# Optimization experiments

Measured on AMD Instinct MI355X. Metric: run time of the kernel, lower is better.

The kernel has to match this reference:

```python
import jax, jax.numpy as jnp
import numpy as np

N, E, B, IN = 20000, 320000, 64, 192


def setup_inputs() -> dict:
    key = jax.random.key(0)
    ks = iter(jax.random.split(key, 80))
    d = {}
    d["x"] = jax.random.normal(next(ks), (N, IN), jnp.float32)
    d["edge_index"] = jax.random.randint(next(ks), (2, E), 0, N - 1)  # +1 shift stays < N
    d["edge_attr"] = jax.random.normal(next(ks), (E,), jnp.float32)
    d["batch"] = jnp.sort(jax.random.randint(next(ks), (N,), 0, B))

    def lin(i, o):
        w = jax.random.normal(next(ks), (i, o), jnp.float32) * (1.0 / i ** 0.5)
        return w, jnp.zeros((o,), jnp.float32)

    dims = [(IN, 4, 64), (256, 4, 64), (256, 6, 32)]  # (in_ch, heads, out_ch) per conv
    for l, (ic, h, c) in enumerate(dims, 1):
        hc = h * c
        d[f"Wq{l}"], d[f"bq{l}"] = lin(ic, hc)
        d[f"Wk{l}"], d[f"bk{l}"] = lin(ic, hc)
        d[f"Wv{l}"], d[f"bv{l}"] = lin(ic, hc)
        d[f"We{l}"] = jax.random.normal(next(ks), (1, hc), jnp.float32)  # lin_edge, no bias
        d[f"Ws{l}"], d[f"bs{l}"] = lin(ic, hc)  # root/skip weight
    d["g1"] = jnp.ones((256,), jnp.float32); d["be1"] = jnp.zeros((256,), jnp.float32)
    d["g2"] = jnp.ones((256,), jnp.float32); d["be2"] = jnp.zeros((256,), jnp.float32)
    d["fc1_w"], d["fc1_b"] = lin(192, 32)
    d["fc2_w"], d["fc2_b"] = lin(32, 2)
    return d


def seg_softmax(s, seg, n):
    # per-destination-node softmax over edges, [E, H]
    m = jax.ops.segment_max(s, seg, num_segments=n)
    m = jnp.where(jnp.isfinite(m), m, 0.0)
    ex = jnp.exp(s - m[seg])
    den = jax.ops.segment_sum(ex, seg, num_segments=n)
    return ex / (den[seg] + 1e-16)


def tconv(x, src, dst, e, Wq, bq, Wk, bk, Wv, bv, We, Ws, bs, h, c):
    # PyG TransformerConv (concat=True, root_weight=True, beta=False, eval -> no dropout)
    n = x.shape[0]
    q = (x @ Wq + bq).reshape(n, h, c)
    k = (x @ Wk + bk).reshape(n, h, c)
    v = (x @ Wv + bv).reshape(n, h, c)
    ee = (e @ We).reshape(-1, h, c)           # [E, h, c] edge embedding
    kj = k[src] + ee                           # gather keys along edges
    scores = jnp.einsum('ehc,ehc->eh', q[dst], kj) * (1.0 / c ** 0.5)
    alpha = seg_softmax(scores, dst, n)        # [E, h]
    msg = (v[src] + ee) * alpha[..., None]
    out = jax.ops.segment_sum(msg, dst, num_segments=n).reshape(n, h * c)
    return out + x @ Ws + bs, alpha


def ln(x, g, b):
    mu = x.mean(-1, keepdims=True)
    var = x.var(-1, keepdims=True)
    return g * (x - mu) / jnp.sqrt(var + 1e-5) + b


def _forward(x, edge_index, edge_attr, batch, Wq1, bq1, Wk1, bk1, Wv1, bv1, We1, Ws1, bs1, Wq2, bq2, Wk2, bk2, Wv2, bv2, We2, Ws2, bs2, Wq3, bq3, Wk3, bk3, Wv3, bv3, We3, Ws3, bs3, g1, be1, g2, be2, fc1_w, fc1_b, fc2_w, fc2_b):
    ei = edge_index + 1                       # replicates `edge_index += 1` in source
    src, dst = ei[0], ei[1]
    e = edge_attr[:, None]                    # edge_dim = 1
    x1, a1 = tconv(x, src, dst, e, Wq1, bq1, Wk1, bk1, Wv1, bv1, We1, Ws1, bs1, 4, 64)
    x1 = jax.nn.relu(ln(x1, g1, be1))
    x2, a2 = tconv(x1, src, dst, e, Wq2, bq2, Wk2, bk2, Wv2, bv2, We2, Ws2, bs2, 4, 64)
    x2 = jax.nn.relu(ln(x2, g2, be2))
    x3, a3 = tconv(x2, src, dst, e, Wq3, bq3, Wk3, bk3, Wv3, bv3, We3, Ws3, bs3, 6, 32)
    x3 = jax.nn.relu(x3)                      # note: norm3 exists in __init__ but is never applied
    xr = x + x3
    cnt = jax.ops.segment_sum(jnp.ones((xr.shape[0],), xr.dtype), batch, num_segments=B)
    pooled = jax.ops.segment_sum(xr, batch, num_segments=B) / jnp.maximum(cnt, 1.0)[:, None]
    h = jax.nn.relu(pooled @ fc1_w + fc1_b)
    logits = h @ fc2_w + fc2_b
    return logits, a1, a2, a3


def reference(x, edge_index, edge_attr, batch, Wq1, bq1, Wk1, bk1, Wv1, bv1, We1, Ws1, bs1, Wq2, bq2, Wk2, bk2, Wv2, bv2, We2, Ws2, bs2, Wq3, bq3, Wk3, bk3, Wv3, bv3, We3, Ws3, bs3, g1, be1, g2, be2, fc1_w, fc1_b, fc2_w, fc2_b):
    return _forward(x, edge_index, edge_attr, batch, Wq1, bq1, Wk1, bk1, Wv1, bv1, We1, Ws1, bs1, Wq2, bq2, Wk2, bk2, Wv2, bv2, We2, Ws2, bs2, Wq3, bq3, Wk3, bk3, Wv3, bv3, We3, Ws3, bs3, g1, be1, g2, be2, fc1_w, fc1_b, fc2_w, fc2_b)
```

## Files before the change

kernel.cpp:

```cpp
#include <hip/hip_runtime.h>
#include <cstdint>
#include <cstddef>

#define DEVINL __device__ __forceinline__

typedef short s16x8 __attribute__((ext_vector_type(8)));
typedef float f32x4 __attribute__((ext_vector_type(4)));
typedef unsigned short u16x4 __attribute__((ext_vector_type(4)));
typedef unsigned short u16x8 __attribute__((ext_vector_type(8)));

DEVINL unsigned short f2bf(float f) {
  unsigned u = __float_as_uint(f);
  unsigned r = (u + 0x7FFFu + ((u >> 16) & 1u)) >> 16;
  return (unsigned short)r;
}
DEVINL float bf2f(unsigned short b) { return __uint_as_float(((unsigned)b) << 16); }

__global__ __launch_bounds__(256) void fill_i32(int* __restrict__ p, int val, int n) {
  int i = blockIdx.x * 256 + threadIdx.x;
  if (i < n) p[i] = val;
}


__global__ __launch_bounds__(256) void cvt_split(const float* __restrict__ in,
                                                 unsigned short* __restrict__ hi,
                                                 unsigned short* __restrict__ lo, int n) {
  int i = blockIdx.x * 256 + threadIdx.x;
  if (i >= n) return;
  float f = in[i];
  unsigned short h = f2bf(f);
  float r = f - bf2f(h);
  hi[i] = h;
  lo[i] = f2bf(r);
}

struct CvtWArgs {
  const float* W[12];
  int K[12];
  int M[12];
};
__global__ __launch_bounds__(256) void cvt_w_all(CvtWArgs a,
                                                 unsigned short* __restrict__ Wh,
                                                 unsigned short* __restrict__ Wl) {
  int tid = blockIdx.x * 256 + threadIdx.x;
  int mat = tid >> 16;
  int off = tid & 65535;
  if (mat >= 12) return;
  int K = a.K[mat], M = a.M[mat];
  if (off >= K * M) return;
  int k = off / M, m = off - k * M;
  float f = a.W[mat][off];
  unsigned short h = f2bf(f);
  float r = f - bf2f(h);
  size_t dst = (size_t)mat * 65536 + (size_t)m * K + k;
  Wh[dst] = h;
  Wl[dst] = f2bf(r);
}

struct GemmArgs {
  const unsigned short* Wh[4];
  const unsigned short* Wl[4];
  const float* bias[4];
  float* out[4];
  int obf[4];
};

template <int KTOT>
__global__ __launch_bounds__(256, 3) void gemm4_lds(
    const unsigned short* __restrict__ Ah, const unsigned short* __restrict__ Al,
    GemmArgs args, int N, int M) {
  const int BK = 64;
  __shared__ unsigned short ash[128 * 64];
  __shared__ unsigned short asl[128 * 64];
  __shared__ unsigned short wsh[64 * 64];
  __shared__ unsigned short wsl[64 * 64];
  int tid = threadIdx.x;
  int wave = tid >> 6, lane = tid & 63;
  int lrow = lane & 15, quad = lane >> 4;
  int mt = M >> 6;
  int z = blockIdx.x / mt;
  int colTile = blockIdx.x - z * mt;
  int row0 = blockIdx.y * 128;
  int col0 = colTile * 64;
  const unsigned short* __restrict__ Wh = args.Wh[z];
  const unsigned short* __restrict__ Wl = args.Wl[z];
  const bool full = (args.obf[z] == 0);

  int ar[4], asq[4];
  size_t agoff[4];
#pragma unroll
  for (int i = 0; i < 4; i++) {
    int c = tid + i * 256;
    ar[i] = c >> 3;
    int kq = c & 7;
    asq[i] = kq ^ (ar[i] & 7);
    int gr = row0 + ar[i]; if (gr >= N) gr = N - 1;
    agoff[i] = (size_t)gr * KTOT + kq * 8;
  }
  int wr[2], wsq[2];
  size_t wgoff[2];
#pragma unroll
  for (int i = 0; i < 2; i++) {
    int c = tid + i * 256;
    wr[i] = c >> 3;
    int kq = c & 7;
    wsq[i] = kq ^ (wr[i] & 7);
    wgoff[i] = (size_t)(col0 + wr[i]) * KTOT + kq * 8;
  }

  s16x8 pa_h[4], pa_l[4], pw_h[2], pw_l[2];
#pragma unroll
  for (int i = 0; i < 4; i++) {
    pa_h[i] = *(const s16x8*)(Ah + agoff[i]);
    pa_l[i] = *(const s16x8*)(Al + agoff[i]);
  }
#pragma unroll
  for (int i = 0; i < 2; i++) {
    pw_h[i] = *(const s16x8*)(Wh + wgoff[i]);
    if (full) pw_l[i] = *(const s16x8*)(Wl + wgoff[i]);
  }

  f32x4 acc[2][4] = {};

  for (int k0 = 0; k0 < KTOT; k0 += BK) {
    __syncthreads();
#pragma unroll
    for (int i = 0; i < 4; i++) {
      *(s16x8*)(ash + ar[i] * 64 + asq[i] * 8) = pa_h[i];
      *(s16x8*)(asl + ar[i] * 64 + asq[i] * 8) = pa_l[i];
    }
#pragma unroll
    for (int i = 0; i < 2; i++) {
      *(s16x8*)(wsh + wr[i] * 64 + wsq[i] * 8) = pw_h[i];
      if (full) *(s16x8*)(wsl + wr[i] * 64 + wsq[i] * 8) = pw_l[i];
    }
    if (k0 + BK < KTOT) {
      int kn = k0 + BK;
#pragma unroll
      for (int i = 0; i < 4; i++) {
        pa_h[i] = *(const s16x8*)(Ah + agoff[i] + kn);
        pa_l[i] = *(const s16x8*)(Al + agoff[i] + kn);
      }
#pragma unroll
      for (int i = 0; i < 2; i++) {
        pw_h[i] = *(const s16x8*)(Wh + wgoff[i] + kn);
        if (full) pw_l[i] = *(const s16x8*)(Wl + wgoff[i] + kn);
      }
    }
    __syncthreads();
#pragma unroll
    for (int kk = 0; kk < 2; kk++) {
      s16x8 fah[2], fal[2], fbh[4], fbl[4];
#pragma unroll
      for (int rf = 0; rf < 2; rf++) {
        int r = wave * 32 + rf * 16 + lrow;
        int sq = (kk * 4 + quad) ^ (lrow & 7);
        fah[rf] = *(const s16x8*)(ash + r * 64 + sq * 8);
        fal[rf] = *(const s16x8*)(asl + r * 64 + sq * 8);
      }
#pragma unroll
      for (int cf = 0; cf < 4; cf++) {
        int cc = cf * 16 + lrow;
        int sq = (kk * 4 + quad) ^ (lrow & 7);
        fbh[cf] = *(const s16x8*)(wsh + cc * 64 + sq * 8);
        if (full) fbl[cf] = *(const s16x8*)(wsl + cc * 64 + sq * 8);
      }
#pragma unroll
      for (int rf = 0; rf < 2; rf++)
#pragma unroll
        for (int cf = 0; cf < 4; cf++) {
          acc[rf][cf] = __builtin_amdgcn_mfma_f32_16x16x32_bf16(fah[rf], fbh[cf], acc[rf][cf], 0, 0, 0);
          acc[rf][cf] = __builtin_amdgcn_mfma_f32_16x16x32_bf16(fal[rf], fbh[cf], acc[rf][cf], 0, 0, 0);
          if (full)
            acc[rf][cf] = __builtin_amdgcn_mfma_f32_16x16x32_bf16(fah[rf], fbl[cf], acc[rf][cf], 0, 0, 0);
        }
    }
  }
  const float* __restrict__ bias = args.bias[z];
  int obf = args.obf[z];
  if (obf == 0) {
    float* __restrict__ C = args.out[z];
#pragma unroll
    for (int cf = 0; cf < 4; cf++) {
      int col = col0 + cf * 16 + lrow;
      float bv = bias[col];
#pragma unroll
      for (int rf = 0; rf < 2; rf++) {
        int rb = row0 + wave * 32 + rf * 16 + quad * 4;
#pragma unroll
        for (int r = 0; r < 4; r++) {
          int rr = rb + r;
          if (rr < N) C[(size_t)rr * M + col] = acc[rf][cf][r] + bv;
        }
      }
    }
  } else {
    __syncthreads();
#pragma unroll
    for (int cf = 0; cf < 4; cf++) {
      int col = cf * 16 + lrow;
      float bv = bias[col0 + col];
#pragma unroll
      for (int rf = 0; rf < 2; rf++) {
        int rl = wave * 32 + rf * 16 + quad * 4;
#pragma unroll
        for (int r = 0; r < 4; r++)
          ash[(rl + r) * 64 + col] = f2bf(acc[rf][cf][r] + bv);
      }
    }
    __syncthreads();
    unsigned short* __restrict__ C = (unsigned short*)args.out[z];
    if (obf == 1) {
#pragma unroll
      for (int i = 0; i < 4; i++) {
        int c = tid + i * 256;
        int row = c >> 3, g8 = c & 7;
        int rr = row0 + row;
        if (rr < N)
          *(u16x8*)(C + (size_t)rr * M + col0 + g8 * 8) =
              *(const u16x8*)(ash + row * 64 + g8 * 8);
      }
    } else {
      int voff = (obf == 3) ? 4 : 0;
      int gbase = col0 >> 2;
#pragma unroll
      for (int i = 0; i < 8; i++) {
        int c = tid + i * 256;
        int row = c >> 4, g4 = c & 15;
        int rr = row0 + row;
        if (rr < N)
          *(u16x4*)(C + (size_t)rr * 2 * M + (size_t)(gbase + g4) * 8 + voff) =
              *(const u16x4*)(ash + row * 64 + g4 * 4);
      }
    }
  }
}


__global__ __launch_bounds__(256) void hist_dst(const int* __restrict__ dst,
                                                int* __restrict__ cnt, int E) {
  int e = blockIdx.x * 256 + threadIdx.x;
  if (e < E) atomicAdd(&cnt[dst[e] + 1], 1);
}

__global__ __launch_bounds__(1024) void scan_hist(const int* __restrict__ cnt,
                                                  int* __restrict__ start,
                                                  int* __restrict__ off, int N) {
  __shared__ int sums[1024];
  const int CH = 20;
  int t = threadIdx.x;
  int base = t * CH;
  int local[CH];
  int tot = 0;
  if (base < N) {
#pragma unroll
    for (int i = 0; i < CH; i++) { local[i] = cnt[base + i]; tot += local[i]; }
  }
  sums[t] = tot;
  __syncthreads();
  for (int d = 1; d < 1024; d <<= 1) {
    int v = (t >= d) ? sums[t - d] : 0;
    __syncthreads();
    sums[t] += v;
    __syncthreads();
  }
  if (base < N) {
    int run = (t == 0) ? 0 : sums[t - 1];
#pragma unroll
    for (int i = 0; i < CH; i++) { start[base + i] = run; off[base + i] = run; run += local[i]; }
    if (base + CH == N) start[N] = run;
  }
}

__global__ __launch_bounds__(256) void scatter_edges(
    const int* __restrict__ src, const int* __restrict__ dst,
    const float* __restrict__ ea, int* __restrict__ off,
    int* __restrict__ src_s, float* __restrict__ ea_s, int* __restrict__ eid_s, int E) {
  int e = blockIdx.x * 256 + threadIdx.x;
  if (e >= E) return;
  int d = dst[e] + 1;
  int pos = atomicAdd(&off[d], 1);
  src_s[pos] = src[e] + 1;
  ea_s[pos] = ea[e];
  eid_s[pos] = e;
}

template <int H, int LPH>
__global__ __launch_bounds__(256) void attn_fused(
    const unsigned short* __restrict__ q, const unsigned short* __restrict__ kv,
    const float* __restrict__ We,
    const int* __restrict__ start, const int* __restrict__ src_s,
    const float* __restrict__ ea_s, const int* __restrict__ eid_s,
    float* __restrict__ sc, float* __restrict__ outp,
    float* __restrict__ alpha, int Nn, float scale) {
  const int HC = H * LPH * 4;
  int w = (blockIdx.x * 256 + threadIdx.x) >> 6;
  int lane = threadIdx.x & 63;
  if (w >= Nn) return;
  int b = start[w], e = start[w + 1];
  if (b == e) return;
  bool act = lane < H * LPH;
  int idx = lane * 4;
  int head = lane / LPH;
  float4 q4 = make_float4(0.f, 0.f, 0.f, 0.f), We4 = q4;
  if (act) {
    u16x4 qv = *(const u16x4*)(q + (size_t)w * HC + idx);
    q4.x = bf2f(qv.x); q4.y = bf2f(qv.y); q4.z = bf2f(qv.z); q4.w = bf2f(qv.w);
    We4 = *(const float4*)(We + idx);
  }
  float qwe = q4.x * We4.x + q4.y * We4.y + q4.z * We4.z + q4.w * We4.w;
#pragma unroll
  for (int mm = 1; mm < LPH; mm <<= 1) qwe += __shfl_xor(qwe, mm, 64);

  float l = 0.f, tv = 0.f;
  float4 accv = make_float4(0.f, 0.f, 0.f, 0.f);

  auto step = [&](u16x8 kvv, float eav, int pos) {
    float p = q4.x * bf2f(kvv[0]) + q4.y * bf2f(kvv[1]) +
              q4.z * bf2f(kvv[2]) + q4.w * bf2f(kvv[3]);
#pragma unroll
    for (int mm = 1; mm < LPH; mm <<= 1) p += __shfl_xor(p, mm, 64);
    float es = __expf((p + eav * qwe) * scale);
    if (act && (lane % LPH) == 0) sc[(size_t)pos * H + head] = es;
    l += es;
    tv = fmaf(es, eav, tv);
    accv.x = fmaf(es, bf2f(kvv[4]), accv.x);
    accv.y = fmaf(es, bf2f(kvv[5]), accv.y);
    accv.z = fmaf(es, bf2f(kvv[6]), accv.z);
    accv.w = fmaf(es, bf2f(kvv[7]), accv.w);
  };

  u16x8 z8 = {0, 0, 0, 0, 0, 0, 0, 0};
  u16x8 kvS[4] = {z8, z8, z8, z8};
  float eaS[4] = {0.f, 0.f, 0.f, 0.f};

  auto preload = [&](int pos, int st) {
    int s = src_s[pos]; eaS[st] = ea_s[pos];
    if (act) kvS[st] = *(const u16x8*)(kv + (size_t)s * 2 * HC + lane * 8);
  };

#pragma unroll
  for (int j = 0; j < 4; j++) if (b + j < e) preload(b + j, j);

  for (int pos = b; pos < e; pos += 4) {
#pragma unroll
    for (int j = 0; j < 4; j++) {
      if (pos + j < e) {
        u16x8 kvc = kvS[j];
        float ec = eaS[j];
        if (pos + j + 4 < e) preload(pos + j + 4, j);
        step(kvc, ec, pos + j);
      }
    }
  }

  float invl = 1.0f / (l + 1e-16f);
  if (act) {
    float* orow = outp + (size_t)w * HC + idx;
    float4 o = *(float4*)orow;
    o.x += (accv.x + tv * We4.x) * invl;
    o.y += (accv.y + tv * We4.y) * invl;
    o.z += (accv.z + tv * We4.z) * invl;
    o.w += (accv.w + tv * We4.w) * invl;
    *(float4*)orow = o;
  }
  {
    int len = e - b;
    const int PCH = 64 / H;
    int p_of = lane / H;
    int h_of = lane - p_of * H;
    float myinv = __shfl(invl, h_of * LPH, 64);
    __threadfence_block();
    for (int base = 0; base < len; base += PCH) {
      int po = base + p_of;
      if (p_of < PCH && po < len) {
        int pos = b + po;
        float es = sc[(size_t)pos * H + h_of];
        alpha[(size_t)eid_s[pos] * H + h_of] = es * myinv;
      }
    }
  }
}


__global__ __launch_bounds__(256) void ln_relu_split(
    const float* __restrict__ in, const float* __restrict__ g,
    const float* __restrict__ b, unsigned short* __restrict__ hi,
    unsigned short* __restrict__ lo, int N) {
  int w = (blockIdx.x * 256 + threadIdx.x) >> 6;
  int lane = threadIdx.x & 63;
  if (w >= N) return;
  float4 x = *(const float4*)(in + (size_t)w * 256 + lane * 4);
  float s = x.x + x.y + x.z + x.w;
  float s2 = x.x * x.x + x.y * x.y + x.z * x.z + x.w * x.w;
  for (int m = 1; m < 64; m <<= 1) { s += __shfl_xor(s, m, 64); s2 += __shfl_xor(s2, m, 64); }
  float mu = s * (1.0f / 256.0f);
  float var = s2 * (1.0f / 256.0f) - mu * mu;
  float inv = rsqrtf(var + 1e-5f);
  float4 gv = *(const float4*)(g + lane * 4);
  float4 bv = *(const float4*)(b + lane * 4);
  float4 y;
  y.x = fmaxf(fmaf((x.x - mu) * inv, gv.x, bv.x), 0.f);
  y.y = fmaxf(fmaf((x.y - mu) * inv, gv.y, bv.y), 0.f);
  y.z = fmaxf(fmaf((x.z - mu) * inv, gv.z, bv.z), 0.f);
  y.w = fmaxf(fmaf((x.w - mu) * inv, gv.w, bv.w), 0.f);
  u16x4 yh, yl;
  yh.x = f2bf(y.x); yl.x = f2bf(y.x - bf2f(yh.x));
  yh.y = f2bf(y.y); yl.y = f2bf(y.y - bf2f(yh.y));
  yh.z = f2bf(y.z); yl.z = f2bf(y.z - bf2f(yh.z));
  yh.w = f2bf(y.w); yl.w = f2bf(y.w - bf2f(yh.w));
  *(u16x4*)(hi + (size_t)w * 256 + lane * 4) = yh;
  *(u16x4*)(lo + (size_t)w * 256 + lane * 4) = yl;
}

__global__ __launch_bounds__(192) void resid_pool2(
    const float* __restrict__ x, const float* __restrict__ x3,
    const int* __restrict__ batch, float* __restrict__ pooled,
    float* __restrict__ cnt, int N, int R) {
  int col = threadIdx.x;
  int r0 = blockIdx.x * R;
  int r1 = min(r0 + R, N);
  if (r0 >= N) return;
  float acc = 0.f;
  int cur = batch[r0];
  int run = 0;
  for (int r = r0; r < r1; r++) {
    int b = batch[r];
    if (b != cur) {
      atomicAdd(&pooled[cur * 192 + col], acc);
      if (col == 0) atomicAdd(&cnt[cur], (float)run);
      acc = 0.f; run = 0; cur = b;
    }
    size_t i = (size_t)r * 192 + col;
    acc += x[i] + fmaxf(x3[i], 0.f);
    run++;
  }
  atomicAdd(&pooled[cur * 192 + col], acc);
  if (col == 0) atomicAdd(&cnt[cur], (float)run);
}

__global__ __launch_bounds__(64) void head_mlp(
    const float* __restrict__ pooled, const float* __restrict__ cnt,
    const float* __restrict__ fc1w, const float* __restrict__ fc1b,
    const float* __restrict__ fc2w, const float* __restrict__ fc2b,
    float* __restrict__ logits) {
  int b = blockIdx.x;
  int t = threadIdx.x;
  __shared__ float p[192];
  __shared__ float hbuf[32];
  float inv = 1.0f / fmaxf(cnt[b], 1.0f);
  for (int i = t; i < 192; i += 64) p[i] = pooled[b * 192 + i] * inv;
  __syncthreads();
  if (t < 32) {
    float acc = fc1b[t];
    for (int i = 0; i < 192; i++) acc = fmaf(p[i], fc1w[i * 32 + t], acc);
    hbuf[t] = fmaxf(acc, 0.f);
  }
  __syncthreads();
  if (t < 2) {
    float acc = fc2b[t];
    for (int j = 0; j < 32; j++) acc = fmaf(hbuf[j], fc2w[j * 2 + t], acc);
    logits[b * 2 + t] = acc;
  }
}

static inline int divup(int a, int b) { return (a + b - 1) / b; }

extern "C" void kernel_launch(void* const* d_in, const int* in_sizes, int n_in,
                              void* d_out, int out_size, void* d_ws, size_t ws_size,
                              hipStream_t stream) {
  const int N = 20000, E = 320000, B = 64;
  const float* x     = (const float*)d_in[0];
  const int*   ei    = (const int*)d_in[1];
  const float* eattr = (const float*)d_in[2];
  const int*   batch = (const int*)d_in[3];
  const int* srcp = ei;
  const int* dstp = ei + E;

  const float* Wq[3]; const float* bq[3]; const float* Wk[3]; const float* bk[3];
  const float* Wv[3]; const float* bv[3]; const float* We[3]; const float* Ws[3];
  const float* bs[3];
  for (int l = 0; l < 3; l++) {
    int base = 4 + l * 9;
    Wq[l] = (const float*)d_in[base + 0]; bq[l] = (const float*)d_in[base + 1];
    Wk[l] = (const float*)d_in[base + 2]; bk[l] = (const float*)d_in[base + 3];
    Wv[l] = (const float*)d_in[base + 4]; bv[l] = (const float*)d_in[base + 5];
    We[l] = (const float*)d_in[base + 6];
    Ws[l] = (const float*)d_in[base + 7]; bs[l] = (const float*)d_in[base + 8];
  }
  const float* g1  = (const float*)d_in[31]; const float* be1 = (const float*)d_in[32];
  const float* g2  = (const float*)d_in[33]; const float* be2 = (const float*)d_in[34];
  const float* fc1w = (const float*)d_in[35]; const float* fc1b = (const float*)d_in[36];
  const float* fc2w = (const float*)d_in[37]; const float* fc2b = (const float*)d_in[38];

  float* out = (float*)d_out;
  float* logits = out;
  float* a1 = out + 128;
  float* a2 = a1 + (size_t)E * 4;
  float* a3 = a2 + (size_t)E * 4;

  float* ws = (float*)d_ws;
  size_t o = 0;
  float* qb = ws + o; o += (size_t)N * 256;
  float* kvb = ws + o; o += (size_t)N * 256;
  float* xa = ws + o; o += (size_t)N * 256;
  float* xb = ws + o; o += (size_t)N * 256;
  float* sc = ws + o; o += (size_t)E * 6;
  int*   cntb  = (int*)(ws + o); o += N;
  int*   startb= (int*)(ws + o); o += N + 1;
  int*   offb  = (int*)(ws + o); o += N + 1;
  int*   src_s = (int*)(ws + o); o += E;
  float* ea_s  = ws + o; o += E;
  int*   eid_s = (int*)(ws + o); o += E;
  float* pooled = ws + o; o += (size_t)B * 192;
  float* cnt    = ws + o; o += B;
  unsigned short* Ah = (unsigned short*)(ws + o); o += (size_t)N * 128;
  unsigned short* Al = (unsigned short*)(ws + o); o += (size_t)N * 128;
  unsigned short* Wh12 = (unsigned short*)(ws + o); o += (size_t)12 * 32768;
  unsigned short* Wl12 = (unsigned short*)(ws + o); o += (size_t)12 * 32768;

  unsigned short* qh  = (unsigned short*)qb;
  unsigned short* kvh = (unsigned short*)kvb;

  dim3 blk(256);

  struct LayerCfg { int K, M; float scale; };
  LayerCfg cfg[3] = {
    {192, 256, 0.125f},
    {256, 256, 0.125f},
    {256, 192, 0.1767766952966369f},
  };
  CvtWArgs cwa;
  for (int l = 0; l < 3; l++) {
    cwa.W[l * 4 + 0] = Wq[l]; cwa.W[l * 4 + 1] = Wk[l];
    cwa.W[l * 4 + 2] = Wv[l]; cwa.W[l * 4 + 3] = Ws[l];
    for (int zz = 0; zz < 4; zz++) {
      cwa.K[l * 4 + zz] = cfg[l].K; cwa.M[l * 4 + zz] = cfg[l].M;
    }
  }
  cvt_w_all<<<12 * 65536 / 256, blk, 0, stream>>>(cwa, Wh12, Wl12);

  fill_i32<<<divup(N, 256), blk, 0, stream>>>(cntb, 0, N);
  hist_dst<<<divup(E, 256), blk, 0, stream>>>(dstp, cntb, E);
  scan_hist<<<1, dim3(1024), 0, stream>>>(cntb, startb, offb, N);
  scatter_edges<<<divup(E, 256), blk, 0, stream>>>(srcp, dstp, eattr, offb,
                                                  src_s, ea_s, eid_s, E);

  float*       lay_out[3] = {xa, xb, xa};
  float*       alpha_out[3] = {a1, a2, a3};

  cvt_split<<<divup(N * 192, 256), blk, 0, stream>>>(x, Ah, Al, N * 192);

  for (int l = 0; l < 3; l++) {
    int M = cfg[l].M;
    GemmArgs ga;
    float* outs[4] = {(float*)qh, (float*)kvh, (float*)kvh, lay_out[l]};
    const float* biases[4] = {bq[l], bk[l], bv[l], bs[l]};
    int obfs[4] = {1, 2, 3, 0};
    for (int z = 0; z < 4; z++) {
      ga.Wh[z] = Wh12 + (size_t)(l * 4 + z) * 65536;
      ga.Wl[z] = Wl12 + (size_t)(l * 4 + z) * 65536;
      ga.bias[z] = biases[z];
      ga.out[z] = outs[z];
      ga.obf[z] = obfs[z];
    }
    dim3 gg((M >> 6) * 4, divup(N, 128));
    if (l == 0)      gemm4_lds<192><<<gg, blk, 0, stream>>>(Ah, Al, ga, N, M);
    else             gemm4_lds<256><<<gg, blk, 0, stream>>>(Ah, Al, ga, N, M);

    dim3 gat(divup(N * 64, 256));
    if (l < 2) {
      attn_fused<4, 16><<<gat, blk, 0, stream>>>(qh, kvh, We[l], startb, src_s,
                                                 ea_s, eid_s, sc, lay_out[l],
                                                 alpha_out[l], N, cfg[l].scale);
    } else {
      attn_fused<6, 8><<<gat, blk, 0, stream>>>(qh, kvh, We[l], startb, src_s,
                                                ea_s, eid_s, sc, lay_out[l],
                                                alpha_out[l], N, cfg[l].scale);
    }
    if (l == 0) ln_relu_split<<<divup(N, 4), blk, 0, stream>>>(xa, g1, be1, Ah, Al, N);
    if (l == 1) ln_relu_split<<<divup(N, 4), blk, 0, stream>>>(xb, g2, be2, Ah, Al, N);
  }

  fill_i32<<<divup(B * 192 + B, 256), blk, 0, stream>>>((int*)pooled, 0, B * 192 + B);
  resid_pool2<<<divup(N, 32), dim3(192), 0, stream>>>(x, xa, batch, pooled, cnt, N, 32);
  head_mlp<<<B, dim3(64), 0, stream>>>(pooled, cnt, fc1w, fc1b, fc2w, fc2b, logits);
}
```

Before: 619.8 us.

## Remap GEMM workgroups per XCD and split interleaved K/V into separate buffers

The GEMM launch becomes a 1D grid whose block ids are remapped so consecutive tiles land on the same XCD, aiming for better L2 reuse of A stripes and weights. K and V projections are now written to separate contiguous bf16 arrays instead of one interleaved buffer, which simplifies the GEMM epilogue to a single store path. The attention kernel does two 8-byte gathers per edge (K and V) instead of one 16-byte gather, which may increase the number of memory transactions per edge.

```diff
diff --git a/kernel.cpp b/kernel.cpp
--- a/kernel.cpp
+++ b/kernel.cpp
@@ -78,9 +78,16 @@
   int wave = tid >> 6, lane = tid & 63;
   int lrow = lane & 15, quad = lane >> 4;
   int mt = M >> 6;
-  int z = blockIdx.x / mt;
-  int colTile = blockIdx.x - z * mt;
-  int row0 = blockIdx.y * 128;
+  int ntile = mt * 4;
+  int id = blockIdx.x, nwg = gridDim.x;
+  int q8 = nwg >> 3, r8 = nwg & 7;
+  int xcd = id & 7, j8 = id >> 3;
+  int wg = (xcd < r8 ? xcd * (q8 + 1) : r8 * (q8 + 1) + (xcd - r8) * q8) + j8;
+  int by = wg / ntile;
+  int bxx = wg - by * ntile;
+  int z = bxx / mt;
+  int colTile = bxx - z * mt;
+  int row0 = by * 128;
   int col0 = colTile * 64;
   const unsigned short* __restrict__ Wh = args.Wh[z];
   const unsigned short* __restrict__ Wl = args.Wl[z];
@@ -210,28 +217,14 @@
     }
     __syncthreads();
     unsigned short* __restrict__ C = (unsigned short*)args.out[z];
-    if (obf == 1) {
-#pragma unroll
-      for (int i = 0; i < 4; i++) {
-        int c = tid + i * 256;
-        int row = c >> 3, g8 = c & 7;
-        int rr = row0 + row;
-        if (rr < N)
-          *(u16x8*)(C + (size_t)rr * M + col0 + g8 * 8) =
-              *(const u16x8*)(ash + row * 64 + g8 * 8);
-      }
-    } else {
-      int voff = (obf == 3) ? 4 : 0;
-      int gbase = col0 >> 2;
-#pragma unroll
-      for (int i = 0; i < 8; i++) {
-        int c = tid + i * 256;
-        int row = c >> 4, g4 = c & 15;
-        int rr = row0 + row;
-        if (rr < N)
-          *(u16x4*)(C + (size_t)rr * 2 * M + (size_t)(gbase + g4) * 8 + voff) =
-              *(const u16x4*)(ash + row * 64 + g4 * 4);
-      }
+#pragma unroll
+    for (int i = 0; i < 4; i++) {
+      int c = tid + i * 256;
+      int row = c >> 3, g8 = c & 7;
+      int rr = row0 + row;
+      if (rr < N)
+        *(u16x8*)(C + (size_t)rr * M + col0 + g8 * 8) =
+            *(const u16x8*)(ash + row * 64 + g8 * 8);
     }
   }
 }
@@ -287,8 +280,8 @@
 
 template <int H, int LPH>
 __global__ __launch_bounds__(256) void attn_fused(
-    const unsigned short* __restrict__ q, const unsigned short* __restrict__ kv,
-    const float* __restrict__ We,
+    const unsigned short* __restrict__ q, const unsigned short* __restrict__ kb,
+    const unsigned short* __restrict__ vb, const float* __restrict__ We,
     const int* __restrict__ start, const int* __restrict__ src_s,
     const float* __restrict__ ea_s, const int* __restrict__ eid_s,
     float* __restrict__ sc, float* __restrict__ outp,
@@ -315,28 +308,32 @@
   float l = 0.f, tv = 0.f;
   float4 accv = make_float4(0.f, 0.f, 0.f, 0.f);
 
-  auto step = [&](u16x8 kvv, float eav, int pos) {
-    float p = q4.x * bf2f(kvv[0]) + q4.y * bf2f(kvv[1]) +
-              q4.z * bf2f(kvv[2]) + q4.w * bf2f(kvv[3]);
+  auto step = [&](u16x4 kc, u16x4 vc, float eav, int pos) {
+    float p = q4.x * bf2f(kc.x) + q4.y * bf2f(kc.y) +
+              q4.z * bf2f(kc.z) + q4.w * bf2f(kc.w);
 #pragma unroll
     for (int mm = 1; mm < LPH; mm <<= 1) p += __shfl_xor(p, mm, 64);
     float es = __expf((p + eav * qwe) * scale);
     if (act && (lane % LPH) == 0) sc[(size_t)pos * H + head] = es;
     l += es;
     tv = fmaf(es, eav, tv);
-    accv.x = fmaf(es, bf2f(kvv[4]), accv.x);
-    accv.y = fmaf(es, bf2f(kvv[5]), accv.y);
-    accv.z = fmaf(es, bf2f(kvv[6]), accv.z);
-    accv.w = fmaf(es, bf2f(kvv[7]), accv.w);
+    accv.x = fmaf(es, bf2f(vc.x), accv.x);
+    accv.y = fmaf(es, bf2f(vc.y), accv.y);
+    accv.z = fmaf(es, bf2f(vc.z), accv.z);
+    accv.w = fmaf(es, bf2f(vc.w), accv.w);
   };
 
-  u16x8 z8 = {0, 0, 0, 0, 0, 0, 0, 0};
-  u16x8 kvS[4] = {z8, z8, z8, z8};
+  u16x4 z4 = {0, 0, 0, 0};
+  u16x4 kS[4] = {z4, z4, z4, z4};
+  u16x4 vS[4] = {z4, z4, z4, z4};
   float eaS[4] = {0.f, 0.f, 0.f, 0.f};
 
   auto preload = [&](int pos, int st) {
     int s = src_s[pos]; eaS[st] = ea_s[pos];
-    if (act) kvS[st] = *(const u16x8*)(kv + (size_t)s * 2 * HC + lane * 8);
+    if (act) {
+      kS[st] = *(const u16x4*)(kb + (size_t)s * HC + idx);
+      vS[st] = *(const u16x4*)(vb + (size_t)s * HC + idx);
+    }
   };
 
 #pragma unroll
@@ -346,10 +343,11 @@
 #pragma unroll
     for (int j = 0; j < 4; j++) {
       if (pos + j < e) {
-        u16x8 kvc = kvS[j];
+        u16x4 kc = kS[j];
+        u16x4 vc = vS[j];
         float ec = eaS[j];
         if (pos + j + 4 < e) preload(pos + j + 4, j);
-        step(kvc, ec, pos + j);
+        step(kc, vc, ec, pos + j);
       }
     }
   }
@@ -519,8 +517,9 @@
   unsigned short* Wh12 = (unsigned short*)(ws + o); o += (size_t)12 * 32768;
   unsigned short* Wl12 = (unsigned short*)(ws + o); o += (size_t)12 * 32768;
 
-  unsigned short* qh  = (unsigned short*)qb;
-  unsigned short* kvh = (unsigned short*)kvb;
+  unsigned short* qh = (unsigned short*)qb;
+  unsigned short* kh = (unsigned short*)kvb;
+  unsigned short* vh = kh + (size_t)N * 256;
 
   dim3 blk(256);
 
@@ -551,12 +550,13 @@
 
   cvt_split<<<divup(N * 192, 256), blk, 0, stream>>>(x, Ah, Al, N * 192);
 
+  int stripes = divup(N, 128);
   for (int l = 0; l < 3; l++) {
     int M = cfg[l].M;
     GemmArgs ga;
-    float* outs[4] = {(float*)qh, (float*)kvh, (float*)kvh, lay_out[l]};
+    float* outs[4] = {(float*)qh, (float*)kh, (float*)vh, lay_out[l]};
     const float* biases[4] = {bq[l], bk[l], bv[l], bs[l]};
-    int obfs[4] = {1, 2, 3, 0};
+    int obfs[4] = {1, 1, 1, 0};
     for (int z = 0; z < 4; z++) {
       ga.Wh[z] = Wh12 + (size_t)(l * 4 + z) * 65536;
       ga.Wl[z] = Wl12 + (size_t)(l * 4 + z) * 65536;
@@ -564,17 +564,17 @@
       ga.out[z] = outs[z];
       ga.obf[z] = obfs[z];
     }
-    dim3 gg((M >> 6) * 4, divup(N, 128));
+    dim3 gg((M >> 6) * 4 * stripes);
     if (l == 0)      gemm4_lds<192><<<gg, blk, 0, stream>>>(Ah, Al, ga, N, M);
     else             gemm4_lds<256><<<gg, blk, 0, stream>>>(Ah, Al, ga, N, M);
 
     dim3 gat(divup(N * 64, 256));
     if (l < 2) {
-      attn_fused<4, 16><<<gat, blk, 0, stream>>>(qh, kvh, We[l], startb, src_s,
+      attn_fused<4, 16><<<gat, blk, 0, stream>>>(qh, kh, vh, We[l], startb, src_s,
                                                  ea_s, eid_s, sc, lay_out[l],
                                                  alpha_out[l], N, cfg[l].scale);
     } else {
-      attn_fused<6, 8><<<gat, blk, 0, stream>>>(qh, kvh, We[l], startb, src_s,
+      attn_fused<6, 8><<<gat, blk, 0, stream>>>(qh, kh, vh, We[l], startb, src_s,
                                                 ea_s, eid_s, sc, lay_out[l],
                                                 alpha_out[l], N, cfg[l].scale);
     }
```

Result: faster. 589.5 us (-4.9%).
